# Kernel tuning notes

Measured on AMD Instinct MI355X. Metric: run time of the kernel, lower is better.

## Reference

```python
import jax, jax.numpy as jnp
import numpy as np

N_NODES = 100000
D = 256
N_EDGES = 1000000
EPS = 1e-8  # torch.cosine_similarity default eps


def setup_inputs() -> dict:
    key = jax.random.key(0)
    ks = jax.random.split(key, 6)
    edge = jax.random.randint(ks[0], (N_EDGES, 2), 0, N_NODES, dtype=jnp.int64)
    emb_matrix0 = jax.random.normal(ks[1], (N_NODES, D), dtype=jnp.float32)
    weight_vec = jax.random.normal(ks[2], (1, D), dtype=jnp.float32)
    W1 = jax.random.normal(ks[3], (64, 2), dtype=jnp.float32) * (6.0 / (2 + 64)) ** 0.5
    b1 = jnp.zeros((64,), dtype=jnp.float32)
    W2 = jax.random.normal(ks[4], (32, 64), dtype=jnp.float32) * (6.0 / (64 + 32)) ** 0.5
    b2 = jnp.zeros((32,), dtype=jnp.float32)
    Wp = jax.random.normal(ks[5], (1, 32), dtype=jnp.float32) * (1.0 / 32) ** 0.5
    bp = jnp.zeros((1,), dtype=jnp.float32)
    return {"edge": edge, "emb_matrix0": emb_matrix0, "weight_vec": weight_vec,
            "W1": W1, "b1": b1, "W2": W2, "b2": b2, "Wp": Wp, "bp": bp}


def reference(edge, emb_matrix0, weight_vec, W1, b1, W2, b2, Wp, bp):
    # Gather two embedding rows per edge and apply the learned per-dim weight.
    x1 = emb_matrix0[edge[:, 0], :] * weight_vec  # [E, D]
    x2 = emb_matrix0[edge[:, 1], :] * weight_vec  # [E, D]
    prod = x1 * x2                                # [E, D]
    dot = jnp.sum(prod, axis=1)                   # [E]
    # torch.cosine_similarity(dim=1): clamp each norm by eps separately.
    n1 = jnp.maximum(jnp.linalg.norm(x1, axis=1), EPS)
    n2 = jnp.maximum(jnp.linalg.norm(x2, axis=1), EPS)
    cos = dot / (n1 * n2)                         # [E]
    interaction = jnp.stack([cos, dot], axis=1)   # [E, 2]
    # Tiny MLP (dropout is identity at inference).
    h = jax.nn.relu(interaction @ W1.T + b1)      # [E, 64]
    h = jax.nn.relu(h @ W2.T + b2)                # [E, 32]
    pred = h @ Wp.T + bp                          # [E, 1]
    return pred.reshape(-1)
```

## Files before the change

kernel.cpp:

```cpp
#include <hip/hip_runtime.h>


#define EPS_COS 1e-8f

constexpr int D = 256;
constexpr int BLOCK = 256;
constexpr int WPB = BLOCK / 64;

typedef _Float16 h2_t __attribute__((ext_vector_type(2)));
typedef _Float16 h8_t __attribute__((ext_vector_type(8)));

#if __has_builtin(__builtin_amdgcn_fdot2)
__device__ inline float fdot2_acc(h2_t a, h2_t b, float c) {
    return __builtin_amdgcn_fdot2(a, b, c, false);
}
#else
__device__ inline float fdot2_acc(h2_t a, h2_t b, float c) {
    return fmaf((float)a[0], (float)b[0], fmaf((float)a[1], (float)b[1], c));
}
#endif

__global__ __launch_bounds__(BLOCK)
void scale_half_kernel(const float* __restrict__ emb,
                       const float* __restrict__ wvec,
                       _Float16* __restrict__ dst, int total8)
{
    const int stride = gridDim.x * blockDim.x;
    for (int i = blockIdx.x * blockDim.x + threadIdx.x; i < total8; i += stride) {
        const float4* src = reinterpret_cast<const float4*>(emb) + (size_t)i * 2;
        float4 a0 = src[0], a1 = src[1];
        const int col8 = i & (D / 8 - 1);
        const float4* w = reinterpret_cast<const float4*>(wvec) + col8 * 2;
        float4 w0 = w[0], w1 = w[1];
        h8_t r;
        r[0] = (_Float16)(a0.x * w0.x); r[1] = (_Float16)(a0.y * w0.y);
        r[2] = (_Float16)(a0.z * w0.z); r[3] = (_Float16)(a0.w * w0.w);
        r[4] = (_Float16)(a1.x * w1.x); r[5] = (_Float16)(a1.y * w1.y);
        r[6] = (_Float16)(a1.z * w1.z); r[7] = (_Float16)(a1.w * w1.w);
        *reinterpret_cast<h8_t*>(dst + (size_t)i * 8) = r;
    }
}

__device__ inline float mlp_eval(float cosv, float dotv,
                                 const float* __restrict__ W1,
                                 const float* __restrict__ b1,
                                 const float* __restrict__ W2,
                                 const float* __restrict__ b2,
                                 const float* __restrict__ Wp,
                                 const float* __restrict__ bp)
{
    float h1[64];
    #pragma unroll
    for (int n = 0; n < 64; ++n)
        h1[n] = fmaxf(fmaf(W1[2 * n], cosv, fmaf(W1[2 * n + 1], dotv, b1[n])), 0.f);
    float pred = bp[0];
    for (int j = 0; j < 32; ++j) {
        const float* w2r = W2 + j * 64;
        float a0 = 0.f, a1 = 0.f, a2 = 0.f, a3 = 0.f;
        #pragma unroll
        for (int k = 0; k < 64; k += 4) {
            a0 = fmaf(w2r[k + 0], h1[k + 0], a0);
            a1 = fmaf(w2r[k + 1], h1[k + 1], a1);
            a2 = fmaf(w2r[k + 2], h1[k + 2], a2);
            a3 = fmaf(w2r[k + 3], h1[k + 3], a3);
        }
        float h2 = fmaxf(b2[j] + ((a0 + a1) + (a2 + a3)), 0.f);
        pred = fmaf(Wp[j], h2, pred);
    }
    return pred;
}

__global__ __launch_bounds__(BLOCK)
void edge_mlp_half_kernel(const int2* __restrict__ edge,
                          const _Float16* __restrict__ tab,
                          const float* __restrict__ W1, const float* __restrict__ b1,
                          const float* __restrict__ W2, const float* __restrict__ b2,
                          const float* __restrict__ Wp, const float* __restrict__ bp,
                          float* __restrict__ out, int E)
{
    __shared__ float2 pairs[WPB][64];

    const int lane  = threadIdx.x & 63;
    const int wslot = threadIdx.x >> 6;
    const int gwid  = blockIdx.x * WPB + wslot;
    const int nwaves = gridDim.x * WPB;
    const int q = lane >> 4;
    const int t = lane & 15;

    const int njobs = (E + 63) >> 6;

    for (int job = gwid; job < njobs; job += nwaves) {
        const int ebase = job << 6;
        const int eidx_mine = ebase + lane;
        int2 eall = (eidx_mine < E) ? edge[eidx_mine] : make_int2(0, 0);

        for (int s = 0; s < 16; ++s) {
            const int src = s * 4 + q;
            const int ex = __shfl(eall.x, src);
            const int ey = __shfl(eall.y, src);
            const uint4* r1 = reinterpret_cast<const uint4*>(tab + (size_t)ex * D) + t;
            const uint4* r2 = reinterpret_cast<const uint4*>(tab + (size_t)ey * D) + t;

            float dotp = 0.f, n1p = 0.f, n2p = 0.f;
            #pragma unroll
            for (int c = 0; c < 2; ++c) {
                uint4 qa = r1[c * 16];
                uint4 qb = r2[c * 16];
                h2_t* pa = reinterpret_cast<h2_t*>(&qa);
                h2_t* pb = reinterpret_cast<h2_t*>(&qb);
                #pragma unroll
                for (int k = 0; k < 4; ++k) {
                    dotp = fdot2_acc(pa[k], pb[k], dotp);
                    n1p  = fdot2_acc(pa[k], pa[k], n1p);
                    n2p  = fdot2_acc(pb[k], pb[k], n2p);
                }
            }
            #pragma unroll
            for (int m = 1; m <= 8; m <<= 1) {
                dotp += __shfl_xor(dotp, m, 16);
                n1p  += __shfl_xor(n1p,  m, 16);
                n2p  += __shfl_xor(n2p,  m, 16);
            }
            if (t == 0) {
                float n1 = fmaxf(sqrtf(n1p), EPS_COS);
                float n2 = fmaxf(sqrtf(n2p), EPS_COS);
                pairs[wslot][src] = make_float2(dotp / (n1 * n2), dotp);
            }
        }

        __builtin_amdgcn_wave_barrier();
        asm volatile("s_waitcnt lgkmcnt(0)" ::: "memory");

        float2 cd = pairs[wslot][lane];
        float pred = mlp_eval(cd.x, cd.y, W1, b1, W2, b2, Wp, bp);

        const int eo = ebase + lane;
        if (eo < E) out[eo] = pred;
    }
}

__global__ __launch_bounds__(BLOCK)
void edge_mlp_f32_kernel(const int2* __restrict__ edge,
                         const float* __restrict__ emb,
                         const float* __restrict__ wvec,
                         const float* __restrict__ W1, const float* __restrict__ b1,
                         const float* __restrict__ W2, const float* __restrict__ b2,
                         const float* __restrict__ Wp, const float* __restrict__ bp,
                         float* __restrict__ out, int E)
{
    __shared__ float2 pairs[WPB][64];
    const int lane  = threadIdx.x & 63;
    const int wslot = threadIdx.x >> 6;
    const int gwid  = blockIdx.x * WPB + wslot;
    const int nwaves = gridDim.x * WPB;
    const int q = lane >> 4;
    const int t = lane & 15;

    float4 wv[4];
    #pragma unroll
    for (int c = 0; c < 4; ++c)
        wv[c] = reinterpret_cast<const float4*>(wvec)[c * 16 + t];

    const int njobs = (E + 63) >> 6;
    for (int job = gwid; job < njobs; job += nwaves) {
        const int ebase = job << 6;
        const int eidx_mine = ebase + lane;
        int2 eall = (eidx_mine < E) ? edge[eidx_mine] : make_int2(0, 0);

        for (int s = 0; s < 16; ++s) {
            const int src = s * 4 + q;
            const int ex = __shfl(eall.x, src);
            const int ey = __shfl(eall.y, src);
            const float4* r1 = reinterpret_cast<const float4*>(emb) + (size_t)ex * (D / 4) + t;
            const float4* r2 = reinterpret_cast<const float4*>(emb) + (size_t)ey * (D / 4) + t;

            float dotp = 0.f, n1p = 0.f, n2p = 0.f;
            #pragma unroll
            for (int c = 0; c < 4; ++c) {
                float4 a = r1[c * 16];
                float4 b = r2[c * 16];
                float4 w = wv[c];
                float x1x = a.x * w.x, x1y = a.y * w.y, x1z = a.z * w.z, x1w = a.w * w.w;
                float x2x = b.x * w.x, x2y = b.y * w.y, x2z = b.z * w.z, x2w = b.w * w.w;
                dotp = fmaf(x1x, x2x, fmaf(x1y, x2y, fmaf(x1z, x2z, fmaf(x1w, x2w, dotp))));
                n1p  = fmaf(x1x, x1x, fmaf(x1y, x1y, fmaf(x1z, x1z, fmaf(x1w, x1w, n1p))));
                n2p  = fmaf(x2x, x2x, fmaf(x2y, x2y, fmaf(x2z, x2z, fmaf(x2w, x2w, n2p))));
            }
            #pragma unroll
            for (int m = 1; m <= 8; m <<= 1) {
                dotp += __shfl_xor(dotp, m, 16);
                n1p  += __shfl_xor(n1p,  m, 16);
                n2p  += __shfl_xor(n2p,  m, 16);
            }
            if (t == 0) {
                float n1 = fmaxf(sqrtf(n1p), EPS_COS);
                float n2 = fmaxf(sqrtf(n2p), EPS_COS);
                pairs[wslot][src] = make_float2(dotp / (n1 * n2), dotp);
            }
        }

        __builtin_amdgcn_wave_barrier();
        asm volatile("s_waitcnt lgkmcnt(0)" ::: "memory");

        float2 cd = pairs[wslot][lane];
        float pred = mlp_eval(cd.x, cd.y, W1, b1, W2, b2, Wp, bp);
        const int eo = ebase + lane;
        if (eo < E) out[eo] = pred;
    }
}

extern "C" void kernel_launch(void* const* d_in, const int* in_sizes, int n_in,
                              void* d_out, int out_size, void* d_ws, size_t ws_size,
                              hipStream_t stream) {
    const int2*  edge = (const int2*)d_in[0];
    const float* emb  = (const float*)d_in[1];
    const float* wvec = (const float*)d_in[2];
    const float* W1   = (const float*)d_in[3];
    const float* b1   = (const float*)d_in[4];
    const float* W2   = (const float*)d_in[5];
    const float* b2   = (const float*)d_in[6];
    const float* Wp   = (const float*)d_in[7];
    const float* bp   = (const float*)d_in[8];
    float* out = (float*)d_out;

    const int E = in_sizes[0] / 2;
    const int emb_elems = in_sizes[1];
    const int njobs = (E + 63) >> 6;
    int nwaves = (njobs + 1) / 2;
    if (nwaves > 8192) nwaves = 8192;
    const int grid_main = (nwaves + WPB - 1) / WPB;

    const size_t need = (size_t)emb_elems * sizeof(_Float16);
    if (ws_size >= need) {
        _Float16* tab = (_Float16*)d_ws;
        const int total8 = emb_elems / 8;
        int cgrid = (total8 + BLOCK - 1) / BLOCK;
        if (cgrid > 2048) cgrid = 2048;
        hipLaunchKernelGGL(scale_half_kernel, dim3(cgrid), dim3(BLOCK), 0, stream,
                           emb, wvec, tab, total8);
        hipLaunchKernelGGL(edge_mlp_half_kernel, dim3(grid_main), dim3(BLOCK), 0, stream,
                           edge, tab, W1, b1, W2, b2, Wp, bp, out, E);
    } else {
        hipLaunchKernelGGL(edge_mlp_f32_kernel, dim3(grid_main), dim3(BLOCK), 0, stream,
                           edge, emb, wvec, W1, b1, W2, b2, Wp, bp, out, E);
    }
}
```

Measured before the change: 325.1 us.

## Quantize scaled embeddings to int8 with per-row scale and use sdot4

Replaces the fp16 scaled embedding table with a per-row symmetric int8 table plus a side array holding each row's scale and inverse norm. The edge kernel computes dot products with integer dot4 and takes the norms from the precomputed side data, so it no longer computes per-edge norms. It also prefetches the next edge pair's rows in software. This halves gather bandwidth and cuts arithmetic, but int8 quantization adds error to dot and cosine values that may exceed tolerance.

```diff
diff --git a/kernel.cpp b/kernel.cpp
--- a/kernel.cpp
+++ b/kernel.cpp
@@ -7,37 +7,73 @@
 constexpr int BLOCK = 256;
 constexpr int WPB = BLOCK / 64;
 
-typedef _Float16 h2_t __attribute__((ext_vector_type(2)));
-typedef _Float16 h8_t __attribute__((ext_vector_type(8)));
-
-#if __has_builtin(__builtin_amdgcn_fdot2)
-__device__ inline float fdot2_acc(h2_t a, h2_t b, float c) {
-    return __builtin_amdgcn_fdot2(a, b, c, false);
-}
+__device__ inline int dot4(int a, int b, int c) {
+#if __has_builtin(__builtin_amdgcn_sdot4)
+    return __builtin_amdgcn_sdot4(a, b, c, false);
 #else
-__device__ inline float fdot2_acc(h2_t a, h2_t b, float c) {
-    return fmaf((float)a[0], (float)b[0], fmaf((float)a[1], (float)b[1], c));
-}
+    c += (int)(signed char)(a)       * (int)(signed char)(b);
+    c += (int)(signed char)(a >> 8)  * (int)(signed char)(b >> 8);
+    c += (int)(signed char)(a >> 16) * (int)(signed char)(b >> 16);
+    c += (int)(signed char)(a >> 24) * (int)(signed char)(b >> 24);
+    return c;
 #endif
+}
 
 __global__ __launch_bounds__(BLOCK)
-void scale_half_kernel(const float* __restrict__ emb,
-                       const float* __restrict__ wvec,
-                       _Float16* __restrict__ dst, int total8)
-{
-    const int stride = gridDim.x * blockDim.x;
-    for (int i = blockIdx.x * blockDim.x + threadIdx.x; i < total8; i += stride) {
-        const float4* src = reinterpret_cast<const float4*>(emb) + (size_t)i * 2;
-        float4 a0 = src[0], a1 = src[1];
-        const int col8 = i & (D / 8 - 1);
-        const float4* w = reinterpret_cast<const float4*>(wvec) + col8 * 2;
-        float4 w0 = w[0], w1 = w[1];
-        h8_t r;
-        r[0] = (_Float16)(a0.x * w0.x); r[1] = (_Float16)(a0.y * w0.y);
-        r[2] = (_Float16)(a0.z * w0.z); r[3] = (_Float16)(a0.w * w0.w);
-        r[4] = (_Float16)(a1.x * w1.x); r[5] = (_Float16)(a1.y * w1.y);
-        r[6] = (_Float16)(a1.z * w1.z); r[7] = (_Float16)(a1.w * w1.w);
-        *reinterpret_cast<h8_t*>(dst + (size_t)i * 8) = r;
+void quant_kernel(const float* __restrict__ emb,
+                  const float* __restrict__ wvec,
+                  unsigned char* __restrict__ qtab,
+                  float2* __restrict__ side,
+                  int N)
+{
+    const int gq = (blockIdx.x * BLOCK + threadIdx.x) >> 4;
+    const int t  = threadIdx.x & 15;
+    if (gq >= N) return;
+
+    const float4* src = reinterpret_cast<const float4*>(emb) + (size_t)gq * 64;
+    const float4* wsc = reinterpret_cast<const float4*>(wvec);
+
+    float p[16];
+    #pragma unroll
+    for (int c = 0; c < 4; ++c) {
+        float4 a = src[4 * t + c];
+        float4 w = wsc[4 * t + c];
+        p[4 * c + 0] = a.x * w.x; p[4 * c + 1] = a.y * w.y;
+        p[4 * c + 2] = a.z * w.z; p[4 * c + 3] = a.w * w.w;
+    }
+
+    float m = 0.f;
+    #pragma unroll
+    for (int i = 0; i < 16; ++i) m = fmaxf(m, fabsf(p[i]));
+    #pragma unroll
+    for (int mask = 1; mask <= 8; mask <<= 1) m = fmaxf(m, __shfl_xor(m, mask, 16));
+
+    const float inv_s = (m > 0.f) ? 127.f / m : 0.f;
+    const float s     = m * (1.f / 127.f);
+
+    float ss = 0.f;
+    unsigned int bw[4];
+    #pragma unroll
+    for (int c = 0; c < 4; ++c) {
+        unsigned int w = 0;
+        #pragma unroll
+        for (int k = 0; k < 4; ++k) {
+            float v = rintf(p[4 * c + k] * inv_s);
+            v = fminf(127.f, fmaxf(-127.f, v));
+            ss = fmaf(v, v, ss);
+            int qv = (int)v;
+            w |= ((unsigned int)(qv & 0xff)) << (8 * k);
+        }
+        bw[c] = w;
+    }
+    *reinterpret_cast<uint4*>(qtab + (size_t)gq * D + t * 16) =
+        make_uint4(bw[0], bw[1], bw[2], bw[3]);
+
+    #pragma unroll
+    for (int mask = 1; mask <= 8; mask <<= 1) ss += __shfl_xor(ss, mask, 16);
+    if (t == 0) {
+        float n = s * sqrtf(ss);
+        side[gq] = make_float2(s, 1.f / fmaxf(n, EPS_COS));
     }
 }
 
@@ -71,12 +107,13 @@
 }
 
 __global__ __launch_bounds__(BLOCK)
-void edge_mlp_half_kernel(const int2* __restrict__ edge,
-                          const _Float16* __restrict__ tab,
-                          const float* __restrict__ W1, const float* __restrict__ b1,
-                          const float* __restrict__ W2, const float* __restrict__ b2,
-                          const float* __restrict__ Wp, const float* __restrict__ bp,
-                          float* __restrict__ out, int E)
+void edge_mlp_i8_kernel(const int2* __restrict__ edge,
+                        const unsigned char* __restrict__ qtab,
+                        const float2* __restrict__ side,
+                        const float* __restrict__ W1, const float* __restrict__ b1,
+                        const float* __restrict__ W2, const float* __restrict__ b2,
+                        const float* __restrict__ Wp, const float* __restrict__ bp,
+                        float* __restrict__ out, int E)
 {
     __shared__ float2 pairs[WPB][64];
 
@@ -94,38 +131,39 @@
         const int eidx_mine = ebase + lane;
         int2 eall = (eidx_mine < E) ? edge[eidx_mine] : make_int2(0, 0);
 
+        int ex = __shfl(eall.x, q);
+        int ey = __shfl(eall.y, q);
+        uint4  qa = reinterpret_cast<const uint4*>(qtab + (size_t)ex * D)[t];
+        uint4  qb = reinterpret_cast<const uint4*>(qtab + (size_t)ey * D)[t];
+        float2 sx = side[ex];
+        float2 sy = side[ey];
+
         for (int s = 0; s < 16; ++s) {
-            const int src = s * 4 + q;
-            const int ex = __shfl(eall.x, src);
-            const int ey = __shfl(eall.y, src);
-            const uint4* r1 = reinterpret_cast<const uint4*>(tab + (size_t)ex * D) + t;
-            const uint4* r2 = reinterpret_cast<const uint4*>(tab + (size_t)ey * D) + t;
-
-            float dotp = 0.f, n1p = 0.f, n2p = 0.f;
+            uint4 nqa = make_uint4(0, 0, 0, 0), nqb = make_uint4(0, 0, 0, 0);
+            float2 nsx = make_float2(0.f, 0.f), nsy = make_float2(0.f, 0.f);
+            if (s < 15) {
+                const int src2 = (s + 1) * 4 + q;
+                const int ex2 = __shfl(eall.x, src2);
+                const int ey2 = __shfl(eall.y, src2);
+                nqa = reinterpret_cast<const uint4*>(qtab + (size_t)ex2 * D)[t];
+                nqb = reinterpret_cast<const uint4*>(qtab + (size_t)ey2 * D)[t];
+                nsx = side[ex2];
+                nsy = side[ey2];
+            }
+
+            int d = 0;
+            d = dot4(qa.x, qb.x, d);
+            d = dot4(qa.y, qb.y, d);
+            d = dot4(qa.z, qb.z, d);
+            d = dot4(qa.w, qb.w, d);
             #pragma unroll
-            for (int c = 0; c < 2; ++c) {
-                uint4 qa = r1[c * 16];
-                uint4 qb = r2[c * 16];
-                h2_t* pa = reinterpret_cast<h2_t*>(&qa);
-                h2_t* pb = reinterpret_cast<h2_t*>(&qb);
-                #pragma unroll
-                for (int k = 0; k < 4; ++k) {
-                    dotp = fdot2_acc(pa[k], pb[k], dotp);
-                    n1p  = fdot2_acc(pa[k], pa[k], n1p);
-                    n2p  = fdot2_acc(pb[k], pb[k], n2p);
-                }
-            }
-            #pragma unroll
-            for (int m = 1; m <= 8; m <<= 1) {
-                dotp += __shfl_xor(dotp, m, 16);
-                n1p  += __shfl_xor(n1p,  m, 16);
-                n2p  += __shfl_xor(n2p,  m, 16);
-            }
-            if (t == 0) {
-                float n1 = fmaxf(sqrtf(n1p), EPS_COS);
-                float n2 = fmaxf(sqrtf(n2p), EPS_COS);
-                pairs[wslot][src] = make_float2(dotp / (n1 * n2), dotp);
-            }
+            for (int mask = 1; mask <= 8; mask <<= 1) d += __shfl_xor(d, mask, 16);
+
+            const float dotf = (float)d * sx.x * sy.x;
+            const float cosv = dotf * sx.y * sy.y;
+            if (t == 0) pairs[wslot][s * 4 + q] = make_float2(cosv, dotf);
+
+            qa = nqa; qb = nqb; sx = nsx; sy = nsy;
         }
 
         __builtin_amdgcn_wave_barrier();
@@ -225,21 +263,23 @@
 
     const int E = in_sizes[0] / 2;
     const int emb_elems = in_sizes[1];
+    const int N = emb_elems / D;
     const int njobs = (E + 63) >> 6;
     int nwaves = (njobs + 1) / 2;
     if (nwaves > 8192) nwaves = 8192;
     const int grid_main = (nwaves + WPB - 1) / WPB;
 
-    const size_t need = (size_t)emb_elems * sizeof(_Float16);
+    const size_t qtab_bytes = ((size_t)emb_elems + 255) & ~(size_t)255;
+    const size_t need = qtab_bytes + (size_t)N * sizeof(float2);
+
     if (ws_size >= need) {
-        _Float16* tab = (_Float16*)d_ws;
-        const int total8 = emb_elems / 8;
-        int cgrid = (total8 + BLOCK - 1) / BLOCK;
-        if (cgrid > 2048) cgrid = 2048;
-        hipLaunchKernelGGL(scale_half_kernel, dim3(cgrid), dim3(BLOCK), 0, stream,
-                           emb, wvec, tab, total8);
-        hipLaunchKernelGGL(edge_mlp_half_kernel, dim3(grid_main), dim3(BLOCK), 0, stream,
-                           edge, tab, W1, b1, W2, b2, Wp, bp, out, E);
+        unsigned char* qtab = (unsigned char*)d_ws;
+        float2* side = (float2*)((char*)d_ws + qtab_bytes);
+        const int qgrid = (N * 16 + BLOCK - 1) / BLOCK;
+        hipLaunchKernelGGL(quant_kernel, dim3(qgrid), dim3(BLOCK), 0, stream,
+                           emb, wvec, qtab, side, N);
+        hipLaunchKernelGGL(edge_mlp_i8_kernel, dim3(grid_main), dim3(BLOCK), 0, stream,
+                           edge, qtab, side, W1, b1, W2, b2, Wp, bp, out, E);
     } else {
         hipLaunchKernelGGL(edge_mlp_f32_kernel, dim3(grid_main), dim3(BLOCK), 0, stream,
                            edge, emb, wvec, W1, b1, W2, b2, Wp, bp, out, E);
```

Result: faster. 272.7 us (-16.1%).
